# Kernel optimization log

Measured on AMD Instinct MI355X. Metric: run time of the kernel, lower is better.

## Reference

```python
import jax, jax.numpy as jnp
import numpy as np

B, T, C = 2, 2048, 2048
NH, G, HS = 16, 4, 128          # heads, kv groups, head dim
QPK = NH // G                    # queries per kv group
K = 4                            # conv kernel width
WIN = 512                        # sliding window (local_window)
SCALE = 1.0 / np.sqrt(HS)


def causal_conv1d_silu(x, w):
    # x: [B, T, D] channels-last, w: [D, K] depthwise kernel; causal left-pad then SiLU
    xp = jnp.pad(x, ((0, 0), (K - 1, 0), (0, 0)))
    out = sum(w[None, None, :, k] * xp[:, k:k + T, :] for k in range(K))
    return jax.nn.silu(out)


def apply_rope(x, cos, sin):
    # x: [B, T, H, HS], cos/sin: [T, HS//2]; non-interleaved halves rotation
    d = cos.shape[-1]
    x1, x2 = x[..., :d], x[..., d:]
    c = cos[None, :, None, :]
    s = sin[None, :, None, :]
    return jnp.concatenate([x1 * c - x2 * s, x1 * s + x2 * c], axis=-1)


def setup_inputs() -> dict:
    key = jax.random.key(0)
    ks = jax.random.split(key, 6)
    x = jax.random.normal(ks[0], (B, T, C), jnp.float32)
    Wqkv = jax.random.normal(ks[1], (C, (NH + 2 * G) * HS), jnp.float32) * 0.02
    Wproj = jax.random.normal(ks[2], (NH * HS, C), jnp.float32) * 0.02
    q_conv_w = jax.random.normal(ks[3], (NH * HS, K), jnp.float32) * 0.3
    k_conv_w = jax.random.normal(ks[4], (G * HS, K), jnp.float32) * 0.3
    v_conv_w = jax.random.normal(ks[5], (G * HS, K), jnp.float32) * 0.3
    # RoPE cache as in build_rope_cache
    theta = 1.0 / (10000.0 ** (jnp.arange(0, HS, 2, dtype=jnp.float32) / HS))
    idx = jnp.outer(jnp.arange(T, dtype=jnp.float32), theta)  # [T, HS//2]
    cos, sin = jnp.cos(idx), jnp.sin(idx)
    return {"x": x, "Wqkv": Wqkv, "Wproj": Wproj,
            "q_conv_w": q_conv_w, "k_conv_w": k_conv_w, "v_conv_w": v_conv_w,
            "cos": cos, "sin": sin}


def reference(x, Wqkv, Wproj, q_conv_w, k_conv_w, v_conv_w, cos, sin):
    # QKV projection + GQA split (group-major head layout, matches torch view/split)
    qkv = (x @ Wqkv).reshape(B, T, G, QPK + 2, HS)
    q = qkv[..., :QPK, :].reshape(B, T, NH * HS)
    k = qkv[..., QPK:QPK + 1, :].reshape(B, T, G * HS)
    v = qkv[..., QPK + 1:, :].reshape(B, T, G * HS)
    # short causal depthwise conv + silu on q/k/v
    q = causal_conv1d_silu(q, q_conv_w).reshape(B, T, NH, HS)
    k = causal_conv1d_silu(k, k_conv_w).reshape(B, T, G, HS)
    v = causal_conv1d_silu(v, v_conv_w).reshape(B, T, G, HS)
    # RoPE
    q = apply_rope(q, cos, sin)
    k = apply_rope(k, cos, sin)
    # expand kv groups to full heads (consecutive repeat matches group-major q)
    k = jnp.repeat(k, QPK, axis=2)  # [B, T, NH, HS]
    v = jnp.repeat(v, QPK, axis=2)
    # sliding-window causal attention
    scores = jnp.einsum('bthd,bshd->bhts', q, k) * SCALE  # [B, NH, T, T]
    i = jnp.arange(T)[:, None]
    j = jnp.arange(T)[None, :]
    mask = (j <= i) & (i - j < WIN)
    scores = jnp.where(mask, scores, jnp.finfo(scores.dtype).min)
    p = jax.nn.softmax(scores, axis=-1)
    y = jnp.einsum('bhts,bshd->bthd', p, v).reshape(B, T, NH * HS)
    return y @ Wproj
```

## Files before the change

### kernel.cpp

```cpp
#include <hip/hip_runtime.h>
#include <math.h>
#include <stdint.h>

#define B_    2
#define T_    2048
#define C_    2048
#define NH_   16
#define G_    4
#define HS_   128
#define WIN_  512
#define NQKV_ 3072
#define M_    4096
#define SCALE_ 0.08838834764831845f

typedef __attribute__((ext_vector_type(8))) __bf16 bf16x8;
typedef __attribute__((ext_vector_type(4))) float f32x4;
typedef unsigned short u16;

static __device__ __forceinline__ u16 f2bf(float f) {
  union { float f; unsigned u; } v; v.f = f;
  unsigned r = v.u + 0x7fffu + ((v.u >> 16) & 1u);
  return (u16)(r >> 16);
}
static __device__ __forceinline__ float bf2f(u16 h) {
  union { unsigned u; float f; } v; v.u = ((unsigned)h) << 16; return v.f;
}
static __device__ __forceinline__ bf16x8 ldg8(const u16* p) {
  return *(const bf16x8*)(const void*)p;
}

__global__ void cvt_bf16(const float* __restrict__ in, u16* __restrict__ out) {
  int i = blockIdx.x * 256 + threadIdx.x;
  float4 v = ((const float4*)in)[i];
  ushort4 o;
  o.x = f2bf(v.x); o.y = f2bf(v.y); o.z = f2bf(v.z); o.w = f2bf(v.w);
  ((ushort4*)out)[i] = o;
}

__global__ void transpose_cvt(const float* __restrict__ in, u16* __restrict__ out,
                              int R, int Ccols) {
  __shared__ float tile[32][33];
  int c0 = blockIdx.x * 32, r0 = blockIdx.y * 32;
  int tx = threadIdx.x & 31, ty = threadIdx.x >> 5;
#pragma unroll
  for (int i = 0; i < 32; i += 8)
    tile[ty + i][tx] = in[(size_t)(r0 + ty + i) * Ccols + c0 + tx];
  __syncthreads();
#pragma unroll
  for (int i = 0; i < 32; i += 8)
    out[(size_t)(c0 + ty + i) * R + r0 + tx] = f2bf(tile[tx][ty + i]);
}

__global__ void transpose_v16(const u16* __restrict__ in, u16* __restrict__ out) {
  __shared__ u16 tile[32][33];
  int b = blockIdx.z;
  int c0 = blockIdx.x * 32, t0 = blockIdx.y * 32;
  int tx = threadIdx.x & 31, ty = threadIdx.x >> 5;
  const u16* src = in + (size_t)b * T_ * (G_*HS_);
  u16* dst = out + (size_t)b * (G_*HS_) * T_;
#pragma unroll
  for (int i = 0; i < 32; i += 8)
    tile[ty + i][tx] = src[(size_t)(t0 + ty + i) * (G_*HS_) + c0 + tx];
  __syncthreads();
#pragma unroll
  for (int i = 0; i < 32; i += 8)
    dst[(size_t)(c0 + ty + i) * T_ + t0 + tx] = tile[tx][ty + i];
}

template<int N, int K, int OUTBF>
__global__ __launch_bounds__(256)
void gemm_bt(const u16* __restrict__ A, const u16* __restrict__ Bt,
             u16* __restrict__ Cb, float* __restrict__ Cf) {
  __shared__ u16 lA[128 * 32];
  __shared__ u16 lB[128 * 32];
  const int m0 = blockIdx.x * 128;
  const int n0 = blockIdx.y * 128;
  const int lane = threadIdx.x & 63;
  const int wave = threadIdx.x >> 6;
  const int wr = (wave >> 1) * 64, wc = (wave & 1) * 64;
  const int fr = lane & 15, fk = (lane >> 4) * 8;
  const int srow = lane >> 2;
  const int scol = (lane & 3) * 8;
  f32x4 acc[4][4] = {};
  for (int k0 = 0; k0 < K; k0 += 32) {
#pragma unroll
    for (int c = 0; c < 2; ++c) {
      int chunk = wave * 2 + c;
      int row = chunk * 16 + srow;
      __builtin_amdgcn_global_load_lds(
          (__attribute__((address_space(1))) void*)(A + (size_t)(m0 + row) * K + k0 + scol),
          (__attribute__((address_space(3))) void*)(lA + chunk * 512), 16, 0, 0);
      __builtin_amdgcn_global_load_lds(
          (__attribute__((address_space(1))) void*)(Bt + (size_t)(n0 + row) * K + k0 + scol),
          (__attribute__((address_space(3))) void*)(lB + chunk * 512), 16, 0, 0);
    }
    __syncthreads();
    bf16x8 af[4], bb[4];
#pragma unroll
    for (int i = 0; i < 4; ++i) {
      af[i] = ldg8(lA + (wr + i * 16 + fr) * 32 + fk);
      bb[i] = ldg8(lB + (wc + i * 16 + fr) * 32 + fk);
    }
#pragma unroll
    for (int i = 0; i < 4; ++i)
#pragma unroll
      for (int j = 0; j < 4; ++j)
        acc[i][j] = __builtin_amdgcn_mfma_f32_16x16x32_bf16(af[i], bb[j], acc[i][j], 0, 0, 0);
    __syncthreads();
  }
  const int orow = m0 + wr + (lane >> 4) * 4;
  const int ocol = n0 + wc + fr;
#pragma unroll
  for (int i = 0; i < 4; ++i)
#pragma unroll
    for (int j = 0; j < 4; ++j)
#pragma unroll
      for (int jj = 0; jj < 4; ++jj) {
        int r = orow + i * 16 + jj, cc = ocol + j * 16;
        if (OUTBF) Cb[(size_t)r * N + cc] = f2bf(acc[i][j][jj]);
        else       Cf[(size_t)r * N + cc] = acc[i][j][jj];
      }
}

static __device__ __forceinline__ float conv_silu(const u16* __restrict__ qkv, int bt, int t,
                                                  int col, const float* __restrict__ w4) {
  float4 w = *(const float4*)w4;
  const u16* p = qkv + (size_t)bt * NQKV_ + col;
  float acc;
  if (t >= 3) {
    acc = w.x * bf2f(p[-3 * NQKV_]) + w.y * bf2f(p[-2 * NQKV_]) +
          w.z * bf2f(p[-1 * NQKV_]) + w.w * bf2f(p[0]);
  } else {
    acc = w.w * bf2f(p[0]);
    if (t >= 1) acc += w.z * bf2f(p[-1 * NQKV_]);
    if (t >= 2) acc += w.y * bf2f(p[-2 * NQKV_]);
  }
  return acc / (1.f + __expf(-acc));
}

__global__ void conv_rope_q(const u16* __restrict__ qkv, const float* __restrict__ w,
                            const float* __restrict__ cosT, const float* __restrict__ sinT,
                            u16* __restrict__ qout) {
  int part = blockIdx.x & 3;
  int bt = blockIdx.x >> 2;
  int t = bt & (T_ - 1);
  int pidx = part * 256 + threadIdx.x;
  int h = pidx >> 6, d = pidx & 63;
  int g = h >> 2, s = h & 3;
  int col = (g * 6 + s) * 128 + d;
  float a1 = conv_silu(qkv, bt, t, col,      w + (size_t)(h * 128 + d) * 4);
  float a2 = conv_silu(qkv, bt, t, col + 64, w + (size_t)(h * 128 + d + 64) * 4);
  float c = cosT[t * 64 + d], sn = sinT[t * 64 + d];
  u16* dst = qout + ((size_t)bt * NH_ + h) * HS_ + d;
  dst[0]  = f2bf((a1 * c - a2 * sn) * SCALE_);
  dst[64] = f2bf((a1 * sn + a2 * c) * SCALE_);
}

__global__ void conv_kv(const u16* __restrict__ qkv, const float* __restrict__ kw,
                        const float* __restrict__ vw, const float* __restrict__ cosT,
                        const float* __restrict__ sinT,
                        u16* __restrict__ kout, u16* __restrict__ vtmp) {
  int bt = blockIdx.x;
  int t = bt & (T_ - 1);
  int g = threadIdx.x >> 6, d = threadIdx.x & 63;
  if (blockIdx.y == 0) {
    int col = (g * 6 + 4) * 128 + d;
    float a1 = conv_silu(qkv, bt, t, col,      kw + (size_t)(g * 128 + d) * 4);
    float a2 = conv_silu(qkv, bt, t, col + 64, kw + (size_t)(g * 128 + d + 64) * 4);
    float c = cosT[t * 64 + d], sn = sinT[t * 64 + d];
    u16* dst = kout + ((size_t)bt * G_ + g) * HS_ + d;
    dst[0]  = f2bf(a1 * c - a2 * sn);
    dst[64] = f2bf(a1 * sn + a2 * c);
  } else {
    int col = (g * 6 + 5) * 128 + d;
    float a1 = conv_silu(qkv, bt, t, col,      vw + (size_t)(g * 128 + d) * 4);
    float a2 = conv_silu(qkv, bt, t, col + 64, vw + (size_t)(g * 128 + d + 64) * 4);
    u16* dst = vtmp + ((size_t)bt * G_ + g) * HS_ + d;
    dst[0]  = f2bf(a1);
    dst[64] = f2bf(a2);
  }
}

__global__ __launch_bounds__(256, 2)
void attn_swin(const u16* __restrict__ qbf, const u16* __restrict__ kbf,
               const u16* __restrict__ vt, u16* __restrict__ ybf) {
  __shared__ __align__(16) char kls[2][16384];
  __shared__ __align__(16) char vls[2][16384];
  __shared__ __align__(16) char pls[4][2048];
  const int lane = threadIdx.x & 63;
  const int wave = threadIdx.x >> 6;
  const int btile = blockIdx.x & 31;
  const int h  = (blockIdx.x >> 5) & 15;
  const int b  = blockIdx.x >> 9;
  const int g  = h >> 2;
  const int t0b = btile << 6;
  const int t0w = t0b + wave * 16;
  const int fr = lane & 15;
  const int hi = lane >> 4;
  const int fko = hi * 8;
  const int qr = t0w + fr;
  char* pl = pls[wave];
  const int swz = (fr & 7) << 4;

  const int krow_l = (lane >> 4);
  const int kcb    = (lane & 15) * 16;
  const int vrow_l = (lane >> 3);
  const int vcb    = (lane & 7) * 16;

  bf16x8 qf[4];
  {
    const u16* qb = qbf + ((size_t)((b * T_ + t0w + fr) * NH_ + h)) * HS_ + fko;
#pragma unroll
    for (int kc = 0; kc < 4; ++kc) qf[kc] = ldg8(qb + kc * 32);
  }

  int sbeg = t0b - (WIN_ - 1); if (sbeg < 0) sbeg = 0; sbeg &= ~63;
  const int nt = (t0b + 64 - sbeg) >> 6;

  const char* kgbase = (const char*)kbf + (((size_t)(b * T_) * G_ + g) * HS_) * 2;
  const char* vgbase = (const char*)vt + ((size_t)(b * (G_*HS_) + g * HS_)) * T_ * 2;

  auto stage = [&](int bufi, int s0) {
    char* kb = kls[bufi]; char* vb = vls[bufi];
#pragma unroll
    for (int c = 0; c < 4; ++c) {
      int i = wave * 4 + c;
      {
        int row = i * 4 + krow_l;
        int scb = kcb ^ ((row & 7) << 4);
        const char* src = kgbase + (size_t)(s0 + row) * (G_*HS_*2) + scb;
        __builtin_amdgcn_global_load_lds(
            (__attribute__((address_space(1))) void*)src,
            (__attribute__((address_space(3))) void*)(kb + i * 1024), 16, 0, 0);
      }
      {
        int row = i * 8 + vrow_l;
        int scb = vcb ^ ((row & 7) << 4);
        const char* src = vgbase + (size_t)row * (T_*2) + (size_t)s0 * 2 + scb;
        __builtin_amdgcn_global_load_lds(
            (__attribute__((address_space(1))) void*)src,
            (__attribute__((address_space(3))) void*)(vb + i * 1024), 16, 0, 0);
      }
    }
  };

  f32x4 acc_o[8];
#pragma unroll
  for (int n = 0; n < 8; ++n) acc_o[n] = (f32x4){0.f, 0.f, 0.f, 0.f};
  float m_r = -1e30f, l_r = 0.f;

  stage(0, sbeg);
  __syncthreads();
  int cur = 0;

  for (int t = 0; t < nt; ++t) {
    int s0 = sbeg + (t << 6);
    if (t + 1 < nt) stage(cur ^ 1, s0 + 64);
    const char* kb = kls[cur];
    const char* vb = vls[cur];

    f32x4 st[4];
    __builtin_amdgcn_s_setprio(1);
#pragma unroll
    for (int c = 0; c < 4; ++c) {
      st[c] = (f32x4){0.f, 0.f, 0.f, 0.f};
      int row = c * 16 + fr;
#pragma unroll
      for (int kc = 0; kc < 4; ++kc) {
        bf16x8 kf = *(const bf16x8*)(kb + row * 256 + ((kc * 64 + hi * 16) ^ swz));
        st[c] = __builtin_amdgcn_mfma_f32_16x16x32_bf16(kf, qf[kc], st[c], 0, 0, 0);
      }
    }
    __builtin_amdgcn_s_setprio(0);

    float tmax = -1e30f;
#pragma unroll
    for (int c = 0; c < 4; ++c)
#pragma unroll
      for (int j = 0; j < 4; ++j) {
        int key = s0 + c * 16 + hi * 4 + j;
        int dlt = qr - key;
        float x = (dlt >= 0 && dlt < WIN_) ? st[c][j] : -1e30f;
        st[c][j] = x;
        tmax = fmaxf(tmax, x);
      }
    tmax = fmaxf(tmax, __shfl_xor(tmax, 16, 64));
    tmax = fmaxf(tmax, __shfl_xor(tmax, 32, 64));
    float mn  = fmaxf(m_r, tmax);
    float fac = __expf(m_r - mn);
    m_r = mn;

    float ps = 0.f;
#pragma unroll
    for (int c = 0; c < 4; ++c) {
      union { ushort4 u4; __bf16 hh[4]; } pk;
#pragma unroll
      for (int j = 0; j < 4; ++j) {
        float p = (st[c][j] > -1e29f) ? __expf(st[c][j] - mn) : 0.f;
        ps += p;
        pk.hh[j] = (__bf16)p;
      }
      *(ushort4*)(pl + fr * 128 + ((c * 32 + hi * 8) ^ swz)) = pk.u4;
    }
    ps += __shfl_xor(ps, 16, 64);
    ps += __shfl_xor(ps, 32, 64);
    l_r = l_r * fac + ps;

    float fq0 = __shfl(fac, hi * 4 + 0, 64);
    float fq1 = __shfl(fac, hi * 4 + 1, 64);
    float fq2 = __shfl(fac, hi * 4 + 2, 64);
    float fq3 = __shfl(fac, hi * 4 + 3, 64);
#pragma unroll
    for (int n = 0; n < 8; ++n) {
      acc_o[n][0] *= fq0; acc_o[n][1] *= fq1;
      acc_o[n][2] *= fq2; acc_o[n][3] *= fq3;
    }

#pragma unroll
    for (int ch = 0; ch < 2; ++ch) {
      bf16x8 pa = *(const bf16x8*)(pl + fr * 128 + ((ch * 64 + hi * 16) ^ swz));
      __builtin_amdgcn_s_setprio(1);
#pragma unroll
      for (int n = 0; n < 8; ++n) {
        int row = n * 16 + fr;
        bf16x8 vf = *(const bf16x8*)(vb + row * 128 + ((ch * 64 + hi * 16) ^ swz));
        acc_o[n] = __builtin_amdgcn_mfma_f32_16x16x32_bf16(pa, vf, acc_o[n], 0, 0, 0);
      }
      __builtin_amdgcn_s_setprio(0);
    }
    __syncthreads();
    cur ^= 1;
  }

  float inv = 1.f / l_r;
  float iq[4];
#pragma unroll
  for (int j = 0; j < 4; ++j) iq[j] = __shfl(inv, hi * 4 + j, 64);
#pragma unroll
  for (int n = 0; n < 8; ++n)
#pragma unroll
    for (int jj = 0; jj < 4; ++jj) {
      int t = t0w + hi * 4 + jj;
      ybf[((size_t)(b * T_ + t)) * (NH_*HS_) + h * HS_ + n * 16 + fr] = f2bf(acc_o[n][jj] * iq[jj]);
    }
}

extern "C" void kernel_launch(void* const* d_in, const int* in_sizes, int n_in,
                              void* d_out, int out_size, void* d_ws, size_t ws_size,
                              hipStream_t stream) {
  (void)in_sizes; (void)n_in; (void)out_size;
  const float* x     = (const float*)d_in[0];
  const float* Wqkv  = (const float*)d_in[1];
  const float* Wproj = (const float*)d_in[2];
  const float* qw    = (const float*)d_in[3];
  const float* kw    = (const float*)d_in[4];
  const float* vw    = (const float*)d_in[5];
  const float* cosT  = (const float*)d_in[6];
  const float* sinT  = (const float*)d_in[7];
  float* out = (float*)d_out;
  char* ws = (char*)d_ws;

  u16* x_bf    = (u16*)(ws + 0);
  u16* wqkv_t  = (u16*)(ws + 16777216);
  u16* wproj_t = (u16*)(ws + 29360128);
  u16* qkv_bf  = (u16*)(ws + 37748736);
  u16* q_bf    = (u16*)(ws + 62914560);
  u16* k_bf    = (u16*)(ws + 79691776);
  u16* v_tmp   = (u16*)(ws + 83886080);
  u16* v_t     = (u16*)(ws + 88080384);
  u16* y_bf    = (u16*)(ws + 92274688);
  if (ws_size < (size_t)109051904) return;

  cvt_bf16<<<8192, 256, 0, stream>>>(x, x_bf);
  transpose_cvt<<<dim3(96, 64), 256, 0, stream>>>(Wqkv, wqkv_t, 2048, 3072);
  transpose_cvt<<<dim3(64, 64), 256, 0, stream>>>(Wproj, wproj_t, 2048, 2048);
  gemm_bt<3072, 2048, 1><<<dim3(32, 24), 256, 0, stream>>>(x_bf, wqkv_t, qkv_bf, nullptr);
  conv_rope_q<<<16384, 256, 0, stream>>>(qkv_bf, qw, cosT, sinT, q_bf);
  conv_kv<<<dim3(4096, 2), 256, 0, stream>>>(qkv_bf, kw, vw, cosT, sinT, k_bf, v_tmp);
  transpose_v16<<<dim3(16, 64, 2), 256, 0, stream>>>(v_tmp, v_t);
  attn_swin<<<1024, 256, 0, stream>>>(q_bf, k_bf, v_t, y_bf);
  gemm_bt<2048, 2048, 0><<<dim3(32, 16), 256, 0, stream>>>(y_bf, wproj_t, nullptr, out);
}
```

Measured before the change: 213.8 us.

## Replace GEMM with 256x256-tile double-buffered swizzled-LDS pipelined kernel

Replaces the 128x128, single-buffered GEMM with a 512-thread 256x256-tile kernel. It double-buffers 64-wide K slices in LDS using global_load_lds with an XOR swizzle, and issues the next stage's loads between the MFMA phases under explicit vmcnt waits and barriers. The goal is to hide global-memory latency behind the matrix math and raise arithmetic intensity per LDS load. The cost is 128KB of LDS per block and fewer blocks: 192 and 128 workgroups, against 256 compute units. That can leave CUs idle and lower occupancy.

```diff
diff --git a/kernel.cpp b/kernel.cpp
--- a/kernel.cpp
+++ b/kernel.cpp
@@ -68,57 +68,112 @@
 }
 
 template<int N, int K, int OUTBF>
-__global__ __launch_bounds__(256)
-void gemm_bt(const u16* __restrict__ A, const u16* __restrict__ Bt,
+__global__ __launch_bounds__(512, 2)
+void gemm256(const u16* __restrict__ A, const u16* __restrict__ Bt,
              u16* __restrict__ Cb, float* __restrict__ Cf) {
-  __shared__ u16 lA[128 * 32];
-  __shared__ u16 lB[128 * 32];
-  const int m0 = blockIdx.x * 128;
-  const int n0 = blockIdx.y * 128;
-  const int lane = threadIdx.x & 63;
-  const int wave = threadIdx.x >> 6;
-  const int wr = (wave >> 1) * 64, wc = (wave & 1) * 64;
-  const int fr = lane & 15, fk = (lane >> 4) * 8;
-  const int srow = lane >> 2;
-  const int scol = (lane & 3) * 8;
-  f32x4 acc[4][4] = {};
-  for (int k0 = 0; k0 < K; k0 += 32) {
-#pragma unroll
-    for (int c = 0; c < 2; ++c) {
-      int chunk = wave * 2 + c;
-      int row = chunk * 16 + srow;
+  __shared__ __align__(16) char lAs[65536];
+  __shared__ __align__(16) char lBs[65536];
+  const int tid  = threadIdx.x;
+  const int lane = tid & 63;
+  const int wave = tid >> 6;
+  const int wm = wave >> 2, wn = wave & 3;
+  const int fr = lane & 15, hi = lane >> 4;
+  const int m0 = blockIdx.x * 256, n0 = blockIdx.y * 256;
+
+  int aoff[8], boff[4];
+#pragma unroll
+  for (int mi = 0; mi < 8; ++mi) {
+    int r = wm * 128 + mi * 16 + fr, P = r >> 1;
+    aoff[mi] = P * 128 + (((((r & 1) << 2) | hi) ^ (P & 7)) << 4);
+  }
+#pragma unroll
+  for (int ni = 0; ni < 4; ++ni) {
+    int r = wn * 64 + ni * 16 + fr, P = r >> 1;
+    boff[ni] = P * 128 + (((((r & 1) << 2) | hi) ^ (P & 7)) << 4);
+  }
+
+  auto stage_half = [&](int S) {
+    int kts = S >> 2, j = S & 3;
+    int kk = j >> 1;
+    const u16* src; int row0; char* base;
+    if (j & 1) { src = Bt; row0 = n0; base = lBs; }
+    else       { src = A;  row0 = m0; base = lAs; }
+    base += ((kts & 1) * 2 + kk) * 16384;
+    int kbase = kts * 64 + kk * 32;
+#pragma unroll
+    for (int i = 0; i < 2; ++i) {
+      int L = i * 512 + tid;
+      int P = L >> 3, c = L & 7;
+      int l = c ^ (P & 7);
+      int r = 2 * P + (l >> 2);
+      const u16* gs = src + (size_t)(row0 + r) * K + kbase + (l & 3) * 8;
       __builtin_amdgcn_global_load_lds(
-          (__attribute__((address_space(1))) void*)(A + (size_t)(m0 + row) * K + k0 + scol),
-          (__attribute__((address_space(3))) void*)(lA + chunk * 512), 16, 0, 0);
-      __builtin_amdgcn_global_load_lds(
-          (__attribute__((address_space(1))) void*)(Bt + (size_t)(n0 + row) * K + k0 + scol),
-          (__attribute__((address_space(3))) void*)(lB + chunk * 512), 16, 0, 0);
-    }
-    __syncthreads();
-    bf16x8 af[4], bb[4];
-#pragma unroll
-    for (int i = 0; i < 4; ++i) {
-      af[i] = ldg8(lA + (wr + i * 16 + fr) * 32 + fk);
-      bb[i] = ldg8(lB + (wc + i * 16 + fr) * 32 + fk);
-    }
-#pragma unroll
-    for (int i = 0; i < 4; ++i)
-#pragma unroll
-      for (int j = 0; j < 4; ++j)
-        acc[i][j] = __builtin_amdgcn_mfma_f32_16x16x32_bf16(af[i], bb[j], acc[i][j], 0, 0, 0);
-    __syncthreads();
-  }
-  const int orow = m0 + wr + (lane >> 4) * 4;
-  const int ocol = n0 + wc + fr;
-#pragma unroll
-  for (int i = 0; i < 4; ++i)
-#pragma unroll
-    for (int j = 0; j < 4; ++j)
+          (__attribute__((address_space(1))) void*)gs,
+          (__attribute__((address_space(3))) void*)(base + L * 16), 16, 0, 0);
+    }
+  };
+
+  f32x4 acc[8][4] = {};
+
+#pragma unroll
+  for (int S = 0; S < 6; ++S) stage_half(S);
+  asm volatile("s_waitcnt vmcnt(8)" ::: "memory");
+  __builtin_amdgcn_s_barrier();
+  asm volatile("" ::: "memory");
+
+  const int NK = K / 64;
+  bf16x8 bcur[4];
+  for (int kt = 0; kt < NK; ++kt) {
+    const char* abase = lAs + (kt & 1) * 32768;
+    const char* bbase = lBs + (kt & 1) * 32768;
+    const bool s01 = kt < NK - 1;
+    const bool s23 = kt < NK - 2;
+#pragma unroll
+    for (int p = 0; p < 4; ++p) {
+      const int kk = p >> 1, wh = p & 1;
+      const char* ab = abase + kk * 16384;
+      const char* bb = bbase + kk * 16384;
+      bf16x8 af[4];
+      if (wh == 0) {
+#pragma unroll
+        for (int ni = 0; ni < 4; ++ni) bcur[ni] = *(const bf16x8*)(bb + boff[ni]);
+      }
+#pragma unroll
+      for (int i = 0; i < 4; ++i) af[i] = *(const bf16x8*)(ab + aoff[wh * 4 + i]);
+      if (p < 2 ? s01 : s23) stage_half(4 * kt + 6 + p);
+      asm volatile("" ::: "memory");
+      __builtin_amdgcn_s_barrier();
+      __builtin_amdgcn_s_setprio(1);
+#pragma unroll
+      for (int i = 0; i < 4; ++i)
+#pragma unroll
+        for (int ni = 0; ni < 4; ++ni)
+          acc[wh * 4 + i][ni] = __builtin_amdgcn_mfma_f32_16x16x32_bf16(
+              af[i], bcur[ni], acc[wh * 4 + i][ni], 0, 0, 0);
+      __builtin_amdgcn_s_setprio(0);
+      if (p == 1) {
+        if (kt == NK - 1) { asm volatile("s_waitcnt vmcnt(0)" ::: "memory"); }
+        else              { asm volatile("s_waitcnt vmcnt(8)" ::: "memory"); }
+      } else if (p == 3) {
+        if (kt < NK - 2)       { asm volatile("s_waitcnt vmcnt(8)" ::: "memory"); }
+        else if (kt == NK - 2) { asm volatile("s_waitcnt vmcnt(4)" ::: "memory"); }
+      }
+      __builtin_amdgcn_s_barrier();
+      asm volatile("" ::: "memory");
+    }
+  }
+
+  const int orow = m0 + wm * 128 + hi * 4;
+  const int ocol = n0 + wn * 64 + fr;
+#pragma unroll
+  for (int mi = 0; mi < 8; ++mi)
+#pragma unroll
+    for (int ni = 0; ni < 4; ++ni)
 #pragma unroll
       for (int jj = 0; jj < 4; ++jj) {
-        int r = orow + i * 16 + jj, cc = ocol + j * 16;
-        if (OUTBF) Cb[(size_t)r * N + cc] = f2bf(acc[i][j][jj]);
-        else       Cf[(size_t)r * N + cc] = acc[i][j][jj];
+        int r = orow + mi * 16 + jj, cc = ocol + ni * 16;
+        if (OUTBF) Cb[(size_t)r * N + cc] = f2bf(acc[mi][ni][jj]);
+        else       Cf[(size_t)r * N + cc] = acc[mi][ni][jj];
       }
 }
 
@@ -374,10 +429,10 @@
   cvt_bf16<<<8192, 256, 0, stream>>>(x, x_bf);
   transpose_cvt<<<dim3(96, 64), 256, 0, stream>>>(Wqkv, wqkv_t, 2048, 3072);
   transpose_cvt<<<dim3(64, 64), 256, 0, stream>>>(Wproj, wproj_t, 2048, 2048);
-  gemm_bt<3072, 2048, 1><<<dim3(32, 24), 256, 0, stream>>>(x_bf, wqkv_t, qkv_bf, nullptr);
+  gemm256<3072, 2048, 1><<<dim3(16, 12), 512, 0, stream>>>(x_bf, wqkv_t, qkv_bf, nullptr);
   conv_rope_q<<<16384, 256, 0, stream>>>(qkv_bf, qw, cosT, sinT, q_bf);
   conv_kv<<<dim3(4096, 2), 256, 0, stream>>>(qkv_bf, kw, vw, cosT, sinT, k_bf, v_tmp);
   transpose_v16<<<dim3(16, 64, 2), 256, 0, stream>>>(v_tmp, v_t);
   attn_swin<<<1024, 256, 0, stream>>>(q_bf, k_bf, v_t, y_bf);
-  gemm_bt<2048, 2048, 0><<<dim3(32, 16), 256, 0, stream>>>(y_bf, wproj_t, nullptr, out);
-}
+  gemm256<2048, 2048, 0><<<dim3(16, 8), 512, 0, stream>>>(y_bf, wproj_t, nullptr, out);
+}
```

After: 229.9 us. 1.08x slower.
